# Kernel optimization log

Measured on AMD Instinct MI355X. Metric: run time of the kernel, lower is better.

## Reference

```python
import jax, jax.numpy as jnp
import numpy as np

B, T, IN, OUT = 32, 128, 512, 512
N, Wd, R, H = 128, 64, 4, 512      # memory slots, word size, read heads, controller size
EPS = 1e-6
IFACE = R * Wd + R + Wd + 1 + Wd + Wd + R + 1 + 1 + 3 * R  # DNC interface vector size


def setup_inputs() -> dict:
    key = jax.random.key(0)
    ks = jax.random.split(key, 6)
    s = jnp.float32(0.05)
    lstm_in = IN + R * Wd
    return {
        "input_sequence": jax.random.normal(ks[0], (B, T, IN), jnp.float32),
        "Wx": jax.random.normal(ks[1], (lstm_in, 4 * H), jnp.float32) * s,
        "Wh": jax.random.normal(ks[2], (H, 4 * H), jnp.float32) * s,
        "b_lstm": jnp.zeros((4 * H,), jnp.float32),
        "W_iface": jax.random.normal(ks[3], (H, IFACE), jnp.float32) * s,
        "b_iface": jnp.zeros((IFACE,), jnp.float32),
        "W_out": jax.random.normal(ks[4], (R * Wd + H, OUT), jnp.float32) * s,
        "b_out": jnp.zeros((OUT,), jnp.float32),
    }


def _alloc(u):
    """DNC allocation weighting for one example. u: [N] usage in [0,1]."""
    phi = jnp.argsort(u)                      # ascending usage (data-dependent gather)
    su = u[phi]
    cp = jnp.cumprod(su)
    cp_excl = jnp.concatenate([jnp.ones((1,), su.dtype), cp[:-1]])
    a_sorted = (1.0 - su) * cp_excl
    return jnp.zeros_like(u).at[phi].set(a_sorted)  # scatter back to original order


def _content(M, keys, beta):
    """Cosine content addressing. M: [B,N,W], keys: [B,K,W], beta: [B,K] -> [B,K,N]."""
    Mn = M / (jnp.linalg.norm(M, axis=-1, keepdims=True) + EPS)
    kn = keys / (jnp.linalg.norm(keys, axis=-1, keepdims=True) + EPS)
    sim = jnp.einsum('bnw,bkw->bkn', Mn, kn)
    return jax.nn.softmax(beta[..., None] * sim, axis=-1)


def _dnc_forward(input_sequence, Wx, Wh, b_lstm, W_iface, b_iface, W_out, b_out):
    eye = 1.0 - jnp.eye(N, dtype=jnp.float32)

    def step(carry, x_t):
        h, c, M, usage, link, prec, ww, wr, reads = carry
        # --- LSTM controller ---
        z = jnp.concatenate([x_t, reads], -1) @ Wx + h @ Wh + b_lstm
        i_g, f_g, g_g, o_g = jnp.split(z, 4, axis=-1)
        c_n = jax.nn.sigmoid(f_g) * c + jax.nn.sigmoid(i_g) * jnp.tanh(g_g)
        h_n = jax.nn.sigmoid(o_g) * jnp.tanh(c_n)
        # --- interface vector ---
        v = h_n @ W_iface + b_iface
        o = [0]
        def take(n):
            out = v[:, o[0]:o[0] + n]; o[0] += n; return out
        read_keys = take(R * Wd).reshape(B, R, Wd)
        read_beta = 1.0 + jax.nn.softplus(take(R))
        write_key = take(Wd).reshape(B, 1, Wd)
        write_beta = 1.0 + jax.nn.softplus(take(1))
        erase = jax.nn.sigmoid(take(Wd))
        write_vec = take(Wd)
        free = jax.nn.sigmoid(take(R))
        alloc_g = jax.nn.sigmoid(take(1))
        write_g = jax.nn.sigmoid(take(1))
        modes = jax.nn.softmax(take(3 * R).reshape(B, R, 3), axis=-1)
        # --- usage & allocation ---
        retention = jnp.prod(1.0 - free[:, :, None] * wr, axis=1)          # [B,N]
        usage_n = (usage + ww - usage * ww) * retention
        a = jax.vmap(_alloc)(usage_n)
        # --- write ---
        cw = _content(M, write_key, write_beta)[:, 0, :]                    # [B,N]
        ww_n = write_g * (alloc_g * a + (1.0 - alloc_g) * cw)
        M_n = M * (1.0 - ww_n[:, :, None] * erase[:, None, :]) + ww_n[:, :, None] * write_vec[:, None, :]
        # --- temporal link ---
        link_n = ((1.0 - ww_n[:, :, None] - ww_n[:, None, :]) * link
                  + ww_n[:, :, None] * prec[:, None, :]) * eye
        prec_n = (1.0 - ww_n.sum(-1, keepdims=True)) * prec + ww_n
        # --- read ---
        fw = jnp.einsum('bij,brj->bri', link_n, wr)
        bw = jnp.einsum('bji,brj->bri', link_n, wr)
        cr = _content(M_n, read_keys, read_beta)
        wr_n = modes[:, :, 0:1] * bw + modes[:, :, 1:2] * cr + modes[:, :, 2:3] * fw
        reads_n = jnp.einsum('brn,bnw->brw', wr_n, M_n).reshape(B, R * Wd)
        # --- output projection ---
        out = jnp.concatenate([reads_n, h_n], -1) @ W_out + b_out
        return (h_n, c_n, M_n, usage_n, link_n, prec_n, ww_n, wr_n, reads_n), out

    f32 = jnp.float32
    init = (jnp.zeros((B, H), f32), jnp.zeros((B, H), f32),
            jnp.zeros((B, N, Wd), f32), jnp.zeros((B, N), f32),
            jnp.zeros((B, N, N), f32), jnp.zeros((B, N), f32),
            jnp.zeros((B, N), f32), jnp.zeros((B, R, N), f32),
            jnp.zeros((B, R * Wd), f32))
    _, outs = jax.lax.scan(step, init, jnp.swapaxes(input_sequence, 0, 1))
    return jnp.swapaxes(outs, 0, 1)  # [B, T, OUT]


def reference(input_sequence, Wx, Wh, b_lstm, W_iface, b_iface, W_out, b_out):
    return _dnc_forward(input_sequence, Wx, Wh, b_lstm, W_iface, b_iface, W_out, b_out)
```

## Files before the change

### kernel.cpp

```cpp
#include <hip/hip_runtime.h>
#include <math.h>

#define TT 128
#define ZD 2048
#define IFC 471
#define EPSF 1e-6f
#define MST 68
#define LST 132
#define NBLK 256
#define UHT 24640
#define VHT 15424

#define FGRP 96
#define NFLAGS 1024

#define D4(a,b) ((a).x*(b).x + (a).y*(b).y + (a).z*(b).z + (a).w*(b).w)

__device__ __forceinline__ float sig_(float x){ return 1.f/(1.f+expf(-x)); }
__device__ __forceinline__ float sp_(float x){ return fmaxf(x,0.f)+log1pf(expf(-fabsf(x))); }

__device__ __forceinline__ void st1(float* p, float v){
  unsigned u; __builtin_memcpy(&u,&v,4);
  __hip_atomic_store((unsigned*)p, u, __ATOMIC_RELAXED, __HIP_MEMORY_SCOPE_AGENT);
}
__device__ __forceinline__ void st2(float* p, float2 v){
  unsigned long long u; __builtin_memcpy(&u,&v,8);
  __hip_atomic_store((unsigned long long*)p, u, __ATOMIC_RELAXED, __HIP_MEMORY_SCOPE_AGENT);
}

__device__ __forceinline__ void arrive(unsigned* f){
  __syncthreads();
  if (threadIdx.x == 0)
    __hip_atomic_fetch_add(f, 1u, __ATOMIC_RELAXED, __HIP_MEMORY_SCOPE_AGENT);
}
__device__ __forceinline__ void wait_ge(const unsigned* f, int n, unsigned gen){
  if (threadIdx.x < 64){
    for (int i = threadIdx.x; i < n; i += 64){
      if (__hip_atomic_load(&f[i], __ATOMIC_RELAXED, __HIP_MEMORY_SCOPE_AGENT) >= gen) continue;
      int spins = 0; bool done = false;
      while (spins < 64){
        if (__hip_atomic_load(&f[i], __ATOMIC_RELAXED, __HIP_MEMORY_SCOPE_AGENT) >= gen){ done = true; break; }
        __builtin_amdgcn_s_sleep(1); ++spins;
      }
      if (!done){
        while (__hip_atomic_load(&f[i], __ATOMIC_RELAXED, __HIP_MEMORY_SCOPE_AGENT) < gen)
          __builtin_amdgcn_s_sleep(8);
      }
    }
  }
  __syncthreads();
}

__device__ __forceinline__ unsigned bf16rne(float f){
  unsigned u; __builtin_memcpy(&u,&f,4);
  return (u + 0x7fffu + ((u>>16)&1u)) >> 16;
}
__device__ __forceinline__ float bflo(unsigned w){
  unsigned u = w << 16; float f; __builtin_memcpy(&f,&u,4); return f;
}
__device__ __forceinline__ float bfhi(unsigned w){
  unsigned u = w & 0xffff0000u; float f; __builtin_memcpy(&f,&u,4); return f;
}

__global__ __launch_bounds__(256) void gemm_bias(
    const float* __restrict__ A, const float* __restrict__ B,
    const float* __restrict__ bias, float* __restrict__ C,
    int Nc, int K)
{
  __shared__ float As[16][68];
  __shared__ float Bs[16][68];
  const int tid = threadIdx.x;
  const int bx = blockIdx.x, by = blockIdx.y;
  const int tx = tid & 15, ty = tid >> 4;
  const int am = tid >> 2, ak = (tid & 3) * 4;
  const int bk = tid >> 4, bn = (tid & 15) * 4;
  float acc[4][4] = {};
  const float* Ap = A + (size_t)(by*64+am)*K + ak;
  const float* Bp = B + (size_t)bk*Nc + bx*64 + bn;
  for (int k0 = 0; k0 < K; k0 += 16) {
    float4 av = *(const float4*)Ap; Ap += 16;
    float4 bv = *(const float4*)Bp; Bp += (size_t)16*Nc;
    As[ak+0][am]=av.x; As[ak+1][am]=av.y; As[ak+2][am]=av.z; As[ak+3][am]=av.w;
    *(float4*)&Bs[bk][bn] = bv;
    __syncthreads();
#pragma unroll
    for (int kk = 0; kk < 16; ++kk) {
      float4 a4 = *(const float4*)&As[kk][ty*4];
      float4 b4 = *(const float4*)&Bs[kk][tx*4];
      acc[0][0]+=a4.x*b4.x; acc[0][1]+=a4.x*b4.y; acc[0][2]+=a4.x*b4.z; acc[0][3]+=a4.x*b4.w;
      acc[1][0]+=a4.y*b4.x; acc[1][1]+=a4.y*b4.y; acc[1][2]+=a4.y*b4.z; acc[1][3]+=a4.y*b4.w;
      acc[2][0]+=a4.z*b4.x; acc[2][1]+=a4.z*b4.y; acc[2][2]+=a4.z*b4.z; acc[2][3]+=a4.z*b4.w;
      acc[3][0]+=a4.w*b4.x; acc[3][1]+=a4.w*b4.y; acc[3][2]+=a4.w*b4.z; acc[3][3]+=a4.w*b4.w;
    }
    __syncthreads();
  }
  float4 bb = *(const float4*)(bias + bx*64 + tx*4);
#pragma unroll
  for (int i = 0; i < 4; ++i) {
    float4 o;
    o.x = acc[i][0]+bb.x; o.y = acc[i][1]+bb.y; o.z = acc[i][2]+bb.z; o.w = acc[i][3]+bb.w;
    *(float4*)(C + (size_t)(by*64+ty*4+i)*Nc + bx*64 + tx*4) = o;
  }
}

__global__ __launch_bounds__(256) void gemm_out(
    const float* __restrict__ A, const float* __restrict__ B,
    const float* __restrict__ bias, float* __restrict__ C)
{
  __shared__ float As[16][68];
  __shared__ float Bs[16][68];
  const int tid = threadIdx.x;
  const int bx = blockIdx.x, by = blockIdx.y;
  const int tx = tid & 15, ty = tid >> 4;
  const int am = tid >> 2, ak = (tid & 3) * 4;
  const int bk = tid >> 4, bn = (tid & 15) * 4;
  float acc[4][4] = {};
  const int arow = by*64 + am;
  const float* Ap = A + (size_t)(arow >> 5)*UHT + (size_t)(arow & 31)*768 + ak;
  const float* Bp = B + (size_t)bk*512 + bx*64 + bn;
  for (int k0 = 0; k0 < 768; k0 += 16) {
    float4 av = *(const float4*)Ap; Ap += 16;
    float4 bv = *(const float4*)Bp; Bp += (size_t)16*512;
    As[ak+0][am]=av.x; As[ak+1][am]=av.y; As[ak+2][am]=av.z; As[ak+3][am]=av.w;
    *(float4*)&Bs[bk][bn] = bv;
    __syncthreads();
#pragma unroll
    for (int kk = 0; kk < 16; ++kk) {
      float4 a4 = *(const float4*)&As[kk][ty*4];
      float4 b4 = *(const float4*)&Bs[kk][tx*4];
      acc[0][0]+=a4.x*b4.x; acc[0][1]+=a4.x*b4.y; acc[0][2]+=a4.x*b4.z; acc[0][3]+=a4.x*b4.w;
      acc[1][0]+=a4.y*b4.x; acc[1][1]+=a4.y*b4.y; acc[1][2]+=a4.y*b4.z; acc[1][3]+=a4.y*b4.w;
      acc[2][0]+=a4.z*b4.x; acc[2][1]+=a4.z*b4.y; acc[2][2]+=a4.z*b4.z; acc[2][3]+=a4.z*b4.w;
      acc[3][0]+=a4.w*b4.x; acc[3][1]+=a4.w*b4.y; acc[3][2]+=a4.w*b4.z; acc[3][3]+=a4.w*b4.w;
    }
    __syncthreads();
  }
  float4 bb = *(const float4*)(bias + bx*64 + tx*4);
#pragma unroll
  for (int i = 0; i < 4; ++i) {
    int row = by*64 + ty*4 + i;
    int crow = (row & 31)*128 + (row >> 5);
    float4 o;
    o.x = acc[i][0]+bb.x; o.y = acc[i][1]+bb.y; o.z = acc[i][2]+bb.z; o.w = acc[i][3]+bb.w;
    *(float4*)(C + (size_t)crow*512 + bx*64 + tx*4) = o;
  }
}

#define SL_L    0
#define SL_M    16896
#define SL_V    25600
#define SL_WR   26080
#define SL_FW   26592
#define SL_BW   27104
#define SL_CR   27616
#define SL_USG  28128
#define SL_PRC  28256
#define SL_WW   28384
#define SL_SU   28512
#define SL_CPX  28640
#define SL_MN   28768
#define SL_SW   28896
#define SL_CW   29024
#define SL_RNK  29152
#define SL_MSC  29280
#define SL_ER   29344
#define SL_WV   29408
#define SL_TOT  29472

#define CWI_U  29564
#define CUS_F  34004
#define CZH_F  37092
#define CCS_F  37396
#define CTOT_F 37548

__global__ void init_flags(unsigned* flags) {
  if (threadIdx.x < NFLAGS)
    __hip_atomic_store(&flags[threadIdx.x], 0u, __ATOMIC_RELAXED, __HIP_MEMORY_SCOPE_AGENT);
}

__global__ __launch_bounds__(1024) void dnc_coop(
    const float* __restrict__ Xproj, const float* __restrict__ Wx,
    const float* __restrict__ Wh, const float* __restrict__ Wif,
    const float* __restrict__ bif,
    float* __restrict__ Uh, float* __restrict__ Vh,
    unsigned* __restrict__ flags)
{
  const int blk = blockIdx.x, tid = threadIdx.x;
  extern __shared__ float sm[];
  const int g = blk & 7;
  const int role = blk >> 3;
  unsigned* FHg = flags + g*FGRP + 0;
  unsigned* FVg = flags + g*FGRP + 32;
  unsigned* FRg = flags + g*FGRP + 64;

  if (role < 4) {
    const int eg = g*4 + role;
    float* L   = sm + SL_L;   float* Ms  = sm + SL_M;
    float* v   = sm + SL_V;   float* wr  = sm + SL_WR;
    float* fw  = sm + SL_FW;  float* bw  = sm + SL_BW;
    float* cr  = sm + SL_CR;  float* usg = sm + SL_USG;
    float* prc = sm + SL_PRC; float* ww  = sm + SL_WW;
    float* su  = sm + SL_SU;  float* cpx = sm + SL_CPX;
    float* Mn  = sm + SL_MN;  float* swv = sm + SL_SW;
    float* cw  = sm + SL_CW;  int*   rnk = (int*)(sm + SL_RNK);
    float* msc = sm + SL_MSC; float* er_ = sm + SL_ER; float* wv_ = sm + SL_WV;

    for (int i = tid; i < SL_TOT; i += 1024) sm[i] = 0.f;
    __syncthreads();

    for (int t = 0; t < TT; ++t) {
      wait_ge(FVg, 28, t+1);
      if (tid < IFC) v[tid] = Vh[(size_t)t*VHT + eg*480 + tid];
      __syncthreads();
      if (tid < 128) {
        float ret = 1.f;
#pragma unroll
        for (int r = 0; r < 4; ++r) { float fr = sig_(v[453+r]); ret *= 1.f - fr*wr[r*128+tid]; }
        float u = usg[tid], w_ = ww[tid];
        usg[tid] = (u + w_ - u*w_) * ret;
      } else if (tid < 256) {
        int n = tid - 128; float nk = 0.f, dot = 0.f;
#pragma unroll
        for (int w = 0; w < 64; w += 4) {
          float4 k4 = *(float4*)&v[260+w];
          float4 m4 = *(float4*)&Ms[n*MST+w];
          nk += D4(k4,k4); dot += D4(m4,k4);
        }
        float beta = 1.f + sp_(v[324]);
        swv[n] = beta * dot / ((Mn[n]+EPSF)*(sqrtf(nk)+EPSF));
      } else if (tid < 260) {
        int r = tid - 256; float s = 0.f;
#pragma unroll
        for (int w = 0; w < 64; w += 4) { float4 k4 = *(float4*)&v[r*64+w]; s += D4(k4,k4); }
        msc[1+r] = sqrtf(s);
      } else if (tid == 260) {
        for (int r = 0; r < 4; ++r) {
          float a0 = v[459+r*3], a1 = v[459+r*3+1], a2 = v[459+r*3+2];
          float mx = fmaxf(a0, fmaxf(a1, a2));
          float e0 = expf(a0-mx), e1 = expf(a1-mx), e2 = expf(a2-mx);
          float dn = e0+e1+e2;
          msc[8+r*3] = e0/dn; msc[8+r*3+1] = e1/dn; msc[8+r*3+2] = e2/dn;
        }
      } else if (tid >= 640 && tid < 704) { int w = tid-640; er_[w] = sig_(v[325+w]); }
      else if (tid >= 704 && tid < 768) { int w = tid-704; wv_[w] = v[389+w]; }
      __syncthreads();
      if (tid < 128) {
        float ui = usg[tid]; int rk = 0;
        for (int j = 0; j < 128; ++j) {
          float uj = usg[j];
          rk += (uj < ui || (uj == ui && j < tid)) ? 1 : 0;
        }
        rnk[tid] = rk; su[rk] = ui;
      } else if (tid < 192) {
        int l = tid - 128;
        float s1 = swv[l], s2 = swv[l+64];
        float m = fmaxf(s1, s2);
#pragma unroll
        for (int o = 32; o > 0; o >>= 1) m = fmaxf(m, __shfl_xor(m, o));
        float e1 = expf(s1-m), e2 = expf(s2-m);
        float dn = e1 + e2;
#pragma unroll
        for (int o = 32; o > 0; o >>= 1) dn += __shfl_xor(dn, o);
        cw[l] = e1/dn; cw[l+64] = e2/dn;
      }
      __syncthreads();
      if (tid < 64) {
        float a0 = su[2*tid], a1 = su[2*tid+1];
        float p = a0*a1, sc = p;
#pragma unroll
        for (int off = 1; off < 64; off <<= 1) {
          float o = __shfl_up(sc, off);
          if ((int)tid >= off) sc *= o;
        }
        float ex = __shfl_up(sc, 1);
        if (tid == 0) ex = 1.f;
        cpx[2*tid] = ex;
        cpx[2*tid+1] = ex*a0;
        float ag = sig_(v[457]), wg = sig_(v[458]);
#pragma unroll
        for (int q = 0; q < 2; ++q) {
          int n = 2*tid + q;
          float a_i = (1.f - usg[n]) * cpx[rnk[n]];
          ww[n] = wg * (ag*a_i + (1.f-ag)*cw[n]);
        }
      }
      __syncthreads();
      {
        int n = tid >> 3, q = tid & 7;
        float wwn = ww[n];
        int w8 = q*8;
#pragma unroll
        for (int gq = 0; gq < 2; ++gq) {
          int w = w8 + gq*4;
          float4 m = *(float4*)&Ms[n*MST+w];
          float4 e4 = *(float4*)&er_[w];
          float4 v4 = *(float4*)&wv_[w];
          m.x = m.x*(1.f - wwn*e4.x) + wwn*v4.x;
          m.y = m.y*(1.f - wwn*e4.y) + wwn*v4.y;
          m.z = m.z*(1.f - wwn*e4.z) + wwn*v4.z;
          m.w = m.w*(1.f - wwn*e4.w) + wwn*v4.w;
          *(float4*)&Ms[n*MST+w] = m;
        }
        int j16 = q*16;
#pragma unroll
        for (int gq = 0; gq < 4; ++gq) {
          int j = j16 + gq*4;
          float4 lv = *(float4*)&L[n*LST + j];
          float4 p4 = *(float4*)&prc[j];
          float4 w4 = *(float4*)&ww[j];
          lv.x = (1.f - wwn - w4.x)*lv.x + wwn*p4.x;
          lv.y = (1.f - wwn - w4.y)*lv.y + wwn*p4.y;
          lv.z = (1.f - wwn - w4.z)*lv.z + wwn*p4.z;
          lv.w = (1.f - wwn - w4.w)*lv.w + wwn*p4.w;
          int d = n - j;
          if (d >= 0 && d < 4) ((float*)&lv)[d] = 0.f;
          *(float4*)&L[n*LST + j] = lv;
        }
      }
      __syncthreads();
      if (tid < 64) {
        float s = ww[tid] + ww[tid+64];
#pragma unroll
        for (int o = 32; o > 0; o >>= 1) s += __shfl_xor(s, o);
        if (tid == 0) msc[0] = s;
      } else if (tid < 192) {
        int n = tid - 64; float s = 0.f;
#pragma unroll
        for (int w = 0; w < 64; w += 4) { float4 m = *(float4*)&Ms[n*MST+w]; s += D4(m,m); }
        Mn[n] = sqrtf(s);
      }
      __syncthreads();
      if (tid < 256) {
        int half = tid >> 7, t2 = tid & 127;
        int i0 = (t2 >> 2) * 4, sg = t2 & 3;
        float4 av[4] = {{0,0,0,0},{0,0,0,0},{0,0,0,0},{0,0,0,0}};
        if (half == 0) {
#pragma unroll
          for (int m = 0; m < 8; ++m) {
            int j = sg*4 + m*16;
            float4 w0 = *(float4*)&wr[0*128+j];
            float4 w1 = *(float4*)&wr[1*128+j];
            float4 w2 = *(float4*)&wr[2*128+j];
            float4 w3 = *(float4*)&wr[3*128+j];
            float4 l0 = *(float4*)&L[(i0+0)*LST+j];
            float4 l1 = *(float4*)&L[(i0+1)*LST+j];
            float4 l2 = *(float4*)&L[(i0+2)*LST+j];
            float4 l3 = *(float4*)&L[(i0+3)*LST+j];
            av[0].x+=D4(l0,w0); av[0].y+=D4(l1,w0); av[0].z+=D4(l2,w0); av[0].w+=D4(l3,w0);
            av[1].x+=D4(l0,w1); av[1].y+=D4(l1,w1); av[1].z+=D4(l2,w1); av[1].w+=D4(l3,w1);
            av[2].x+=D4(l0,w2); av[2].y+=D4(l1,w2); av[2].z+=D4(l2,w2); av[2].w+=D4(l3,w2);
            av[3].x+=D4(l0,w3); av[3].y+=D4(l1,w3); av[3].z+=D4(l2,w3); av[3].w+=D4(l3,w3);
          }
        } else {
#pragma unroll
          for (int m = 0; m < 32; ++m) {
            int j = sg + m*4;
            float4 lv = *(float4*)&L[j*LST + i0];
            float w0 = wr[j], w1 = wr[128+j], w2 = wr[256+j], w3 = wr[384+j];
            av[0].x+=w0*lv.x; av[0].y+=w0*lv.y; av[0].z+=w0*lv.z; av[0].w+=w0*lv.w;
            av[1].x+=w1*lv.x; av[1].y+=w1*lv.y; av[1].z+=w1*lv.z; av[1].w+=w1*lv.w;
            av[2].x+=w2*lv.x; av[2].y+=w2*lv.y; av[2].z+=w2*lv.z; av[2].w+=w2*lv.w;
            av[3].x+=w3*lv.x; av[3].y+=w3*lv.y; av[3].z+=w3*lv.z; av[3].w+=w3*lv.w;
          }
        }
#pragma unroll
        for (int r = 0; r < 4; ++r) {
          av[r].x += __shfl_xor(av[r].x,1); av[r].x += __shfl_xor(av[r].x,2);
          av[r].y += __shfl_xor(av[r].y,1); av[r].y += __shfl_xor(av[r].y,2);
          av[r].z += __shfl_xor(av[r].z,1); av[r].z += __shfl_xor(av[r].z,2);
          av[r].w += __shfl_xor(av[r].w,1); av[r].w += __shfl_xor(av[r].w,2);
        }
        if (sg == 0) {
          float* dst = half ? bw : fw;
#pragma unroll
          for (int r = 0; r < 4; ++r) {
            dst[r*128 + i0+0] = av[r].x; dst[r*128 + i0+1] = av[r].y;
            dst[r*128 + i0+2] = av[r].z; dst[r*128 + i0+3] = av[r].w;
          }
        }
      } else if (tid < 384) {
        int n = tid - 256;
        prc[n] = (1.f - msc[0])*prc[n] + ww[n];
      } else if (tid >= 512) {
        int r = (tid >> 7) & 3, n = tid & 127;
        float dot = 0.f;
#pragma unroll
        for (int w = 0; w < 64; w += 4) {
          float4 m4 = *(float4*)&Ms[n*MST+w];
          float4 k4 = *(float4*)&v[r*64+w];
          dot += D4(m4,k4);
        }
        float beta = 1.f + sp_(v[256+r]);
        cr[r*128+n] = beta * dot / ((Mn[n]+EPSF)*(msc[1+r]+EPSF));
      }
      __syncthreads();
      if (tid < 256) {
        int r = tid >> 6, l = tid & 63;
        float s1 = cr[r*128+l], s2 = cr[r*128+l+64];
        float m = fmaxf(s1, s2);
#pragma unroll
        for (int o = 32; o > 0; o >>= 1) m = fmaxf(m, __shfl_xor(m, o));
        float e1 = expf(s1-m), e2 = expf(s2-m);
        float dn = e1 + e2;
#pragma unroll
        for (int o = 32; o > 0; o >>= 1) dn += __shfl_xor(dn, o);
        float m0 = msc[8+r*3], m1 = msc[8+r*3+1], m2 = msc[8+r*3+2];
        wr[r*128+l]    = m0*bw[r*128+l]    + m1*(e1/dn) + m2*fw[r*128+l];
        wr[r*128+l+64] = m0*bw[r*128+l+64] + m1*(e2/dn) + m2*fw[r*128+l+64];
      }
      __syncthreads();
      if (tid < 512) {
        int r = tid >> 7, t2 = tid & 127;
        int w0 = (t2 >> 3) * 4, ns = t2 & 7;
        float4 a = {0,0,0,0};
#pragma unroll
        for (int m = 0; m < 16; ++m) {
          int n = ns + m*8;
          float4 mr = *(float4*)&Ms[n*MST + w0];
          float wv = wr[r*128 + n];
          a.x += wv*mr.x; a.y += wv*mr.y; a.z += wv*mr.z; a.w += wv*mr.w;
        }
        a.x += __shfl_xor(a.x,1); a.x += __shfl_xor(a.x,2); a.x += __shfl_xor(a.x,4);
        a.y += __shfl_xor(a.y,1); a.y += __shfl_xor(a.y,2); a.y += __shfl_xor(a.y,4);
        a.z += __shfl_xor(a.z,1); a.z += __shfl_xor(a.z,2); a.z += __shfl_xor(a.z,4);
        a.w += __shfl_xor(a.w,1); a.w += __shfl_xor(a.w,2); a.w += __shfl_xor(a.w,4);
        if (ns == 0) {
          int o = r*64 + w0;
          float2 lo = {a.x, a.y}, hi = {a.z, a.w};
          st2(&Uh[(size_t)t*UHT + eg*768 + o], lo);
          st2(&Uh[(size_t)t*UHT + eg*768 + o + 2], hi);
        }
      }
      arrive(&FRg[role]);
    }
  } else {
    const int c = role - 4;
    const int egB = g*4;
    const int d0 = (512*c)/28, d1 = (512*(c+1))/28, Dd = d1-d0, NJ = 4*Dd;
    const int v0 = (471*c)/28, v1 = (471*(c+1))/28, JV = v1-v0;
    unsigned* Wzu = (unsigned*)sm;
    unsigned* Wiu = (unsigned*)sm + CWI_U;
    float* us  = sm + CUS_F;
    float* zh  = sm + CZH_F;
    float* cst = sm + CCS_F;

    for (int idx = tid; idx < NJ*384; idx += 1024) {
      int j = idx/384, p = idx - j*384, k = 2*p;
      int q = j/Dd, di = j - q*Dd, gc = q*512 + d0 + di;
      float w0 = (k < 256) ? Wx[(size_t)(512+k)*ZD + gc] : Wh[(size_t)(k-256)*ZD + gc];
      float w1 = (k+1 < 256) ? Wx[(size_t)(513+k)*ZD + gc] : Wh[(size_t)(k-255)*ZD + gc];
      Wzu[j*389 + p] = bf16rne(w0) | (bf16rne(w1) << 16);
    }
    for (int idx = tid; idx < JV*256; idx += 1024) {
      int j = idx/256, p = idx - j*256, k = 2*p, gc = v0 + j;
      float w0 = Wif[(size_t)k*IFC + gc];
      float w1 = Wif[(size_t)(k+1)*IFC + gc];
      Wiu[j*261 + p] = bf16rne(w0) | (bf16rne(w1) << 16);
    }
    if (tid < 76) cst[tid] = 0.f;
    if (tid < 4*NJ) {
      int e = tid/NJ, j = tid - e*NJ;
      int q = j/Dd, di = j - q*Dd, gc = q*512 + d0 + di;
      zh[e*76 + j] = Xproj[((size_t)(egB+e)*TT + 0)*ZD + gc];
    }
    __syncthreads();
    if (tid < 4*Dd) {
      int e = tid/Dd, di = tid - e*Dd;
      float zi = zh[e*76 + di], zg = zh[e*76 + 2*Dd + di], zo = zh[e*76 + 3*Dd + di];
      float cn = sig_(zi)*tanhf(zg);
      float hn = sig_(zo)*tanhf(cn);
      cst[tid] = cn;
      st1(&Uh[(size_t)0*UHT + (egB + e)*768 + 256 + d0 + di], hn);
    }
    arrive(&FHg[c]);

    for (int t = 0; t < TT; ++t) {
      wait_ge(FHg, 28, t+1);
      if (tid < 512) {
        int e = tid >> 7, f4 = (tid & 127) * 4;
        *(float4*)&us[e*772 + 256 + f4] =
            *(const float4*)&Uh[(size_t)t*UHT + (egB+e)*768 + 256 + f4];
      }
      if (t+1 < TT && tid < 4*NJ) {
        int e = tid/NJ, j = tid - e*NJ;
        int q = j/Dd, di = j - q*Dd, gc = q*512 + d0 + di;
        zh[e*76 + j] = Xproj[((size_t)(egB+e)*TT + t+1)*ZD + gc];
      }
      __syncthreads();
      if (tid < 544) {
        int g8 = tid >> 3, ks = tid & 7;
        int e = g8/17, j = g8 - e*17;
        if (j < JV) {
          float acc = 0.f;
#pragma unroll 4
          for (int m = 0; m < 32; ++m) {
            int p = m*8 + ks;
            float2 hv = *(const float2*)&us[e*772 + 256 + 2*p];
            unsigned wu = Wiu[j*261 + p];
            acc += hv.x*bflo(wu) + hv.y*bfhi(wu);
          }
          acc += __shfl_xor(acc,1); acc += __shfl_xor(acc,2); acc += __shfl_xor(acc,4);
          if (ks == 0) {
            int col = v0 + j;
            st1(&Vh[(size_t)t*VHT + (egB+e)*480 + col], bif[col] + acc);
          }
        }
      }
      arrive(&FVg[c]);
      if (t+1 < TT) {
        if (tid < 608) {
          int q2 = tid >> 1, ks = tid & 1;
          int e = q2/76, j = q2 - e*76;
          if (j < NJ) {
            float acc = 0.f;
#pragma unroll 4
            for (int m = 0; m < 128; ++m) {
              int pp = m*2 + ks;
              float2 hv = *(const float2*)&us[e*772 + 256 + 2*pp];
              unsigned wu = Wzu[j*389 + 128 + pp];
              acc += hv.x*bflo(wu) + hv.y*bfhi(wu);
            }
            acc += __shfl_xor(acc,1);
            if (ks == 0) zh[e*76 + j] += acc;
          }
        }
        wait_ge(FRg, 4, t+1);
        if (tid < 256) {
          int e = tid >> 6, f4 = (tid & 63) * 4;
          *(float4*)&us[e*772 + f4] =
              *(const float4*)&Uh[(size_t)t*UHT + (egB+e)*768 + f4];
        }
        __syncthreads();
        if (tid < 608) {
          int q2 = tid >> 1, ks = tid & 1;
          int e = q2/76, j = q2 - e*76;
          if (j < NJ) {
            float acc = 0.f;
#pragma unroll 4
            for (int m = 0; m < 64; ++m) {
              int pp = m*2 + ks;
              float2 rv = *(const float2*)&us[e*772 + 2*pp];
              unsigned wu = Wzu[j*389 + pp];
              acc += rv.x*bflo(wu) + rv.y*bfhi(wu);
            }
            acc += __shfl_xor(acc,1);
            if (ks == 0) zh[e*76 + j] += acc;
          }
        }
        __syncthreads();
        if (tid < 4*Dd) {
          int e = tid/Dd, di = tid - e*Dd;
          float zi = zh[e*76 + di],      zf = zh[e*76 + Dd + di];
          float zg = zh[e*76 + 2*Dd+di], zo = zh[e*76 + 3*Dd + di];
          float cn = sig_(zf)*cst[tid] + sig_(zi)*tanhf(zg);
          float hn = sig_(zo)*tanhf(cn);
          cst[tid] = cn;
          st1(&Uh[(size_t)(t+1)*UHT + (egB+e)*768 + 256 + d0 + di], hn);
        }
        arrive(&FHg[c]);
      }
    }
  }
}

extern "C" void kernel_launch(void* const* d_in, const int* in_sizes, int n_in,
                              void* d_out, int out_size, void* d_ws, size_t ws_size,
                              hipStream_t stream) {
  const float* x   = (const float*)d_in[0];
  const float* Wx  = (const float*)d_in[1];
  const float* Wh  = (const float*)d_in[2];
  const float* bl  = (const float*)d_in[3];
  const float* Wif = (const float*)d_in[4];
  const float* bif = (const float*)d_in[5];
  const float* Wo  = (const float*)d_in[6];
  const float* bo  = (const float*)d_in[7];
  float* out = (float*)d_out;

  float* Xp = (float*)d_ws;
  float* Uh = Xp + (size_t)4096*2048;
  float* Vh = Uh + (size_t)TT*UHT;
  unsigned* fl = (unsigned*)(Vh + (size_t)TT*VHT);

  gemm_bias<<<dim3(2048/64, 4096/64), dim3(256), 0, stream>>>(x, Wx, bl, Xp, 2048, 512);

  init_flags<<<dim3(1), dim3(NFLAGS), 0, stream>>>(fl);

  const int smem_bytes = CTOT_F * 4;
  (void)hipFuncSetAttribute((const void*)dnc_coop, hipFuncAttributeMaxDynamicSharedMemorySize, smem_bytes);
  void* args[] = { (void*)&Xp, (void*)&Wx, (void*)&Wh, (void*)&Wif, (void*)&bif,
                   (void*)&Uh, (void*)&Vh, (void*)&fl };
  (void)hipLaunchCooperativeKernel((void*)dnc_coop, dim3(NBLK), dim3(1024), args,
                                   (unsigned int)smem_bytes, stream);

  gemm_out<<<dim3(512/64, 4096/64), dim3(256), 0, stream>>>(Uh, Wo, bo, out);
}
```

Before: 4.204 ms.

## Shrink LDS row padding, use float2 accesses, prefetch Xproj before flag wait

Reduces the shared-memory row strides for the memory matrix and link matrix from 68/132 to 66/130 and recomputes the LDS slot offsets. All float4 LDS accesses on these arrays become paired float2 accesses, because the new strides only keep rows 8-byte aligned. The spin-wait sleep in the inter-block barrier is shortened, and the next-step Xproj load is issued before waiting on the flag so its latency overlaps the wait. The intent is fewer LDS bank conflicts, lower barrier wake-up latency and hidden global load latency, at the cost of twice as many LDS instructions and more polling traffic.

New measurement: 4.221 ms. Within noise of the previous version (+0.4%).

```diff
diff --git a/kernel.cpp b/kernel.cpp
--- a/kernel.cpp
+++ b/kernel.cpp
@@ -5,8 +5,8 @@
 #define ZD 2048
 #define IFC 471
 #define EPSF 1e-6f
-#define MST 68
-#define LST 132
+#define MST 66
+#define LST 130
 #define NBLK 256
 #define UHT 24640
 #define VHT 15424
@@ -44,7 +44,7 @@
       }
       if (!done){
         while (__hip_atomic_load(&f[i], __ATOMIC_RELAXED, __HIP_MEMORY_SCOPE_AGENT) < gen)
-          __builtin_amdgcn_s_sleep(8);
+          __builtin_amdgcn_s_sleep(2);
       }
     }
   }
@@ -147,25 +147,25 @@
 }
 
 #define SL_L    0
-#define SL_M    16896
-#define SL_V    25600
-#define SL_WR   26080
-#define SL_FW   26592
-#define SL_BW   27104
-#define SL_CR   27616
-#define SL_USG  28128
-#define SL_PRC  28256
-#define SL_WW   28384
-#define SL_SU   28512
-#define SL_CPX  28640
-#define SL_MN   28768
-#define SL_SW   28896
-#define SL_CW   29024
-#define SL_RNK  29152
-#define SL_MSC  29280
-#define SL_ER   29344
-#define SL_WV   29408
-#define SL_TOT  29472
+#define SL_M    16640
+#define SL_V    25088
+#define SL_WR   25568
+#define SL_FW   26080
+#define SL_BW   26592
+#define SL_CR   27104
+#define SL_USG  27616
+#define SL_PRC  27744
+#define SL_WW   27872
+#define SL_SU   28000
+#define SL_CPX  28128
+#define SL_MN   28256
+#define SL_SW   28384
+#define SL_CW   28512
+#define SL_RNK  28640
+#define SL_MSC  28768
+#define SL_ER   28832
+#define SL_WV   28896
+#define SL_TOT  28960
 
 #define CWI_U  29564
 #define CUS_F  34004
@@ -221,10 +221,10 @@
       } else if (tid < 256) {
         int n = tid - 128; float nk = 0.f, dot = 0.f;
 #pragma unroll
-        for (int w = 0; w < 64; w += 4) {
-          float4 k4 = *(float4*)&v[260+w];
-          float4 m4 = *(float4*)&Ms[n*MST+w];
-          nk += D4(k4,k4); dot += D4(m4,k4);
+        for (int w = 0; w < 64; w += 2) {
+          float2 k2 = *(float2*)&v[260+w];
+          float2 m2 = *(float2*)&Ms[n*MST+w];
+          nk += k2.x*k2.x + k2.y*k2.y; dot += m2.x*k2.x + m2.y*k2.y;
         }
         float beta = 1.f + sp_(v[324]);
         swv[n] = beta * dot / ((Mn[n]+EPSF)*(sqrtf(nk)+EPSF));
@@ -290,31 +290,28 @@
         float wwn = ww[n];
         int w8 = q*8;
 #pragma unroll
-        for (int gq = 0; gq < 2; ++gq) {
-          int w = w8 + gq*4;
-          float4 m = *(float4*)&Ms[n*MST+w];
-          float4 e4 = *(float4*)&er_[w];
-          float4 v4 = *(float4*)&wv_[w];
-          m.x = m.x*(1.f - wwn*e4.x) + wwn*v4.x;
-          m.y = m.y*(1.f - wwn*e4.y) + wwn*v4.y;
-          m.z = m.z*(1.f - wwn*e4.z) + wwn*v4.z;
-          m.w = m.w*(1.f - wwn*e4.w) + wwn*v4.w;
-          *(float4*)&Ms[n*MST+w] = m;
+        for (int gq = 0; gq < 4; ++gq) {
+          int w = w8 + gq*2;
+          float2 m = *(float2*)&Ms[n*MST+w];
+          float2 e2 = *(float2*)&er_[w];
+          float2 v2 = *(float2*)&wv_[w];
+          m.x = m.x*(1.f - wwn*e2.x) + wwn*v2.x;
+          m.y = m.y*(1.f - wwn*e2.y) + wwn*v2.y;
+          *(float2*)&Ms[n*MST+w] = m;
         }
         int j16 = q*16;
 #pragma unroll
-        for (int gq = 0; gq < 4; ++gq) {
-          int j = j16 + gq*4;
-          float4 lv = *(float4*)&L[n*LST + j];
-          float4 p4 = *(float4*)&prc[j];
-          float4 w4 = *(float4*)&ww[j];
-          lv.x = (1.f - wwn - w4.x)*lv.x + wwn*p4.x;
-          lv.y = (1.f - wwn - w4.y)*lv.y + wwn*p4.y;
-          lv.z = (1.f - wwn - w4.z)*lv.z + wwn*p4.z;
-          lv.w = (1.f - wwn - w4.w)*lv.w + wwn*p4.w;
+        for (int gq = 0; gq < 8; ++gq) {
+          int j = j16 + gq*2;
+          float2 lv = *(float2*)&L[n*LST + j];
+          float2 p2 = *(float2*)&prc[j];
+          float2 w2 = *(float2*)&ww[j];
+          lv.x = (1.f - wwn - w2.x)*lv.x + wwn*p2.x;
+          lv.y = (1.f - wwn - w2.y)*lv.y + wwn*p2.y;
           int d = n - j;
-          if (d >= 0 && d < 4) ((float*)&lv)[d] = 0.f;
-          *(float4*)&L[n*LST + j] = lv;
+          if (d == 0) lv.x = 0.f;
+          if (d == 1) lv.y = 0.f;
+          *(float2*)&L[n*LST + j] = lv;
         }
       }
       __syncthreads();
@@ -326,7 +323,7 @@
       } else if (tid < 192) {
         int n = tid - 64; float s = 0.f;
 #pragma unroll
-        for (int w = 0; w < 64; w += 4) { float4 m = *(float4*)&Ms[n*MST+w]; s += D4(m,m); }
+        for (int w = 0; w < 64; w += 2) { float2 m = *(float2*)&Ms[n*MST+w]; s += m.x*m.x + m.y*m.y; }
         Mn[n] = sqrtf(s);
       }
       __syncthreads();
@@ -342,25 +339,31 @@
             float4 w1 = *(float4*)&wr[1*128+j];
             float4 w2 = *(float4*)&wr[2*128+j];
             float4 w3 = *(float4*)&wr[3*128+j];
-            float4 l0 = *(float4*)&L[(i0+0)*LST+j];
-            float4 l1 = *(float4*)&L[(i0+1)*LST+j];
-            float4 l2 = *(float4*)&L[(i0+2)*LST+j];
-            float4 l3 = *(float4*)&L[(i0+3)*LST+j];
-            av[0].x+=D4(l0,w0); av[0].y+=D4(l1,w0); av[0].z+=D4(l2,w0); av[0].w+=D4(l3,w0);
-            av[1].x+=D4(l0,w1); av[1].y+=D4(l1,w1); av[1].z+=D4(l2,w1); av[1].w+=D4(l3,w1);
-            av[2].x+=D4(l0,w2); av[2].y+=D4(l1,w2); av[2].z+=D4(l2,w2); av[2].w+=D4(l3,w2);
-            av[3].x+=D4(l0,w3); av[3].y+=D4(l1,w3); av[3].z+=D4(l2,w3); av[3].w+=D4(l3,w3);
+#pragma unroll
+            for (int k = 0; k < 4; ++k) {
+              float2 la = *(float2*)&L[(i0+k)*LST+j];
+              float2 lb = *(float2*)&L[(i0+k)*LST+j+2];
+              float dv0 = la.x*w0.x + la.y*w0.y + lb.x*w0.z + lb.y*w0.w;
+              float dv1 = la.x*w1.x + la.y*w1.y + lb.x*w1.z + lb.y*w1.w;
+              float dv2 = la.x*w2.x + la.y*w2.y + lb.x*w2.z + lb.y*w2.w;
+              float dv3 = la.x*w3.x + la.y*w3.y + lb.x*w3.z + lb.y*w3.w;
+              if (k == 0){ av[0].x+=dv0; av[1].x+=dv1; av[2].x+=dv2; av[3].x+=dv3; }
+              if (k == 1){ av[0].y+=dv0; av[1].y+=dv1; av[2].y+=dv2; av[3].y+=dv3; }
+              if (k == 2){ av[0].z+=dv0; av[1].z+=dv1; av[2].z+=dv2; av[3].z+=dv3; }
+              if (k == 3){ av[0].w+=dv0; av[1].w+=dv1; av[2].w+=dv2; av[3].w+=dv3; }
+            }
           }
         } else {
 #pragma unroll
           for (int m = 0; m < 32; ++m) {
             int j = sg + m*4;
-            float4 lv = *(float4*)&L[j*LST + i0];
+            float2 la = *(float2*)&L[j*LST + i0];
+            float2 lb = *(float2*)&L[j*LST + i0 + 2];
             float w0 = wr[j], w1 = wr[128+j], w2 = wr[256+j], w3 = wr[384+j];
-            av[0].x+=w0*lv.x; av[0].y+=w0*lv.y; av[0].z+=w0*lv.z; av[0].w+=w0*lv.w;
-            av[1].x+=w1*lv.x; av[1].y+=w1*lv.y; av[1].z+=w1*lv.z; av[1].w+=w1*lv.w;
-            av[2].x+=w2*lv.x; av[2].y+=w2*lv.y; av[2].z+=w2*lv.z; av[2].w+=w2*lv.w;
-            av[3].x+=w3*lv.x; av[3].y+=w3*lv.y; av[3].z+=w3*lv.z; av[3].w+=w3*lv.w;
+            av[0].x+=w0*la.x; av[0].y+=w0*la.y; av[0].z+=w0*lb.x; av[0].w+=w0*lb.y;
+            av[1].x+=w1*la.x; av[1].y+=w1*la.y; av[1].z+=w1*lb.x; av[1].w+=w1*lb.y;
+            av[2].x+=w2*la.x; av[2].y+=w2*la.y; av[2].z+=w2*lb.x; av[2].w+=w2*lb.y;
+            av[3].x+=w3*la.x; av[3].y+=w3*la.y; av[3].z+=w3*lb.x; av[3].w+=w3*lb.y;
           }
         }
 #pragma unroll
@@ -385,10 +388,10 @@
         int r = (tid >> 7) & 3, n = tid & 127;
         float dot = 0.f;
 #pragma unroll
-        for (int w = 0; w < 64; w += 4) {
-          float4 m4 = *(float4*)&Ms[n*MST+w];
-          float4 k4 = *(float4*)&v[r*64+w];
-          dot += D4(m4,k4);
+        for (int w = 0; w < 64; w += 2) {
+          float2 m2 = *(float2*)&Ms[n*MST+w];
+          float2 k2 = *(float2*)&v[r*64+w];
+          dot += m2.x*k2.x + m2.y*k2.y;
         }
         float beta = 1.f + sp_(v[256+r]);
         cr[r*128+n] = beta * dot / ((Mn[n]+EPSF)*(msc[1+r]+EPSF));
@@ -416,9 +419,10 @@
 #pragma unroll
         for (int m = 0; m < 16; ++m) {
           int n = ns + m*8;
-          float4 mr = *(float4*)&Ms[n*MST + w0];
+          float2 ma = *(float2*)&Ms[n*MST + w0];
+          float2 mb = *(float2*)&Ms[n*MST + w0 + 2];
           float wv = wr[r*128 + n];
-          a.x += wv*mr.x; a.y += wv*mr.y; a.z += wv*mr.z; a.w += wv*mr.w;
+          a.x += wv*ma.x; a.y += wv*ma.y; a.z += wv*mb.x; a.w += wv*mb.y;
         }
         a.x += __shfl_xor(a.x,1); a.x += __shfl_xor(a.x,2); a.x += __shfl_xor(a.x,4);
         a.y += __shfl_xor(a.y,1); a.y += __shfl_xor(a.y,2); a.y += __shfl_xor(a.y,4);
@@ -475,6 +479,12 @@
     arrive(&FHg[c]);
 
     for (int t = 0; t < TT; ++t) {
+      float xpre = 0.f; int pe = 0, pj = 0;
+      if (t+1 < TT && tid < 4*NJ) {
+        pe = tid/NJ; pj = tid - pe*NJ;
+        int q = pj/Dd, di = pj - q*Dd, gc = q*512 + d0 + di;
+        xpre = Xproj[((size_t)(egB+pe)*TT + t+1)*ZD + gc];
+      }
       wait_ge(FHg, 28, t+1);
       if (tid < 512) {
         int e = tid >> 7, f4 = (tid & 127) * 4;
@@ -482,9 +492,7 @@
             *(const float4*)&Uh[(size_t)t*UHT + (egB+e)*768 + 256 + f4];
       }
       if (t+1 < TT && tid < 4*NJ) {
-        int e = tid/NJ, j = tid - e*NJ;
-        int q = j/Dd, di = j - q*Dd, gc = q*512 + d0 + di;
-        zh[e*76 + j] = Xproj[((size_t)(egB+e)*TT + t+1)*ZD + gc];
+        zh[pe*76 + pj] = xpre;
       }
       __syncthreads();
       if (tid < 544) {
```
